# Optimization experiments

Measured on AMD Instinct MI355X. Metric: run time of the kernel, lower is better.

Reference implementation:

```python
import math
import jax, jax.numpy as jnp
import numpy as np

S = 32.0
M1 = 1.0
M2 = 0.5
M3 = 0.0
MM = M2 * math.sin(math.pi - M2)
NUM_CLASSES = 100000
FEATURES = 512
BATCH = 512


def setup_inputs() -> dict:
    key = jax.random.key(0)
    k1, k2, k3 = jax.random.split(key, 3)
    inputs = jax.random.normal(k1, (BATCH, FEATURES), dtype=jnp.float32)
    labels = jax.random.randint(k2, (BATCH,), 0, NUM_CLASSES, dtype=jnp.int64)
    # xavier_uniform on [num_classes, features]
    limit = math.sqrt(6.0 / (NUM_CLASSES + FEATURES))
    weight = jax.random.uniform(k3, (NUM_CLASSES, FEATURES), minval=-limit, maxval=limit, dtype=jnp.float32)
    return {"inputs": inputs, "labels": labels, "weight": weight}


def reference(inputs, labels, weight):
    # L2 normalize (torch F.normalize uses eps=1e-12 clamp on norm)
    inp_n = inputs / jnp.maximum(jnp.linalg.norm(inputs, axis=1, keepdims=True), 1e-12)
    w_n = weight / jnp.maximum(jnp.linalg.norm(weight, axis=1, keepdims=True), 1e-12)
    cos_in = jnp.clip(inp_n @ w_n.T, -1.0 + 1e-6, 1.0 - 1e-6)  # [N, C]
    theta_in = jnp.arccos(cos_in)
    one_hot = jax.nn.one_hot(labels, NUM_CLASSES, dtype=cos_in.dtype)
    theta_out = theta_in + (theta_in * (M1 - 1.0) + M2) * one_hot
    cos_out = jnp.where(
        theta_out < math.pi,
        jnp.cos(theta_out) - M3 * one_hot,
        cos_in - MM * one_hot - M3 * one_hot,
    )
    outs = S * cos_out  # [N, C]
    # mean cross-entropy
    logp = jax.nn.log_softmax(outs, axis=1)
    n = jnp.arange(BATCH)
    loss = -jnp.mean(logp[n, labels])
    target_cos_in = cos_in[n, labels][:, None]
    target_theta_in = theta_in[n, labels][:, None]
    target_cos_out = cos_out[n, labels][:, None]
    return loss, outs, target_cos_in, target_theta_in, target_cos_out
```

## Files before the change

### kernel.cpp

```cpp
#include <hip/hip_runtime.h>
#include <stdint.h>

#define BATCH 512
#define FEAT 512
#define NCLS 100000
#define BM 128
#define BN 128
#define BK 64
#define NBLK_N 782
#define NBLK (NBLK_N * 4)
#define NCHUNK (NBLK_N * 2)
#define SCALE_S 32.0f
#define MARGIN 0.5f
#define MM_CONST 0.23971276930210156f
#define PI_F 3.14159265358979f

typedef unsigned int u32;
typedef unsigned short u16;
typedef __bf16 bf16x8 __attribute__((ext_vector_type(8)));
typedef float f32x4 __attribute__((ext_vector_type(4)));

__device__ __forceinline__ u16 f2bf(float f) {
  u32 u = __float_as_uint(f);
  u += 0x7fffu + ((u >> 16) & 1u);
  return (u16)(u >> 16);
}

__device__ __forceinline__ void async_copy16(const void* g, void* l) {
  __builtin_amdgcn_global_load_lds((const __attribute__((address_space(1))) u32*)g,
                                   (__attribute__((address_space(3))) u32*)l,
                                   16, 0, 0);
}

__device__ __forceinline__ float block_reduce_sum(float v, float* sbuf) {
  for (int off = 1; off < 64; off <<= 1) v += __shfl_xor(v, off, 64);
  int wid = threadIdx.x >> 6, lane = threadIdx.x & 63;
  __syncthreads();
  if (lane == 0) sbuf[wid] = v;
  __syncthreads();
  return sbuf[0] + sbuf[1] + sbuf[2] + sbuf[3];
}

__global__ __launch_bounds__(256) void norm_all_kernel(const float* __restrict__ inputs,
                                                       const float* __restrict__ weight,
                                                       u16* __restrict__ dstA,
                                                       u16* __restrict__ dstB) {
  const int lane = threadIdx.x & 63;
  const int gw = (blockIdx.x * 256 + threadIdx.x) >> 6;
  const int nw = gridDim.x * 4;
  for (int row = gw; row < BATCH + NCLS; row += nw) {
    const float* src;
    u16* dst;
    if (row < BATCH) {
      src = inputs + (size_t)row * FEAT;
      dst = dstA + (size_t)row * FEAT;
    } else {
      src = weight + (size_t)(row - BATCH) * FEAT;
      dst = dstB + (size_t)(row - BATCH) * FEAT;
    }
    const float4* p4 = (const float4*)src;
    float4 a = p4[lane];
    float4 b = p4[lane + 64];
    float ss = a.x * a.x + a.y * a.y + a.z * a.z + a.w * a.w +
               b.x * b.x + b.y * b.y + b.z * b.z + b.w * b.w;
#pragma unroll
    for (int off = 1; off < 64; off <<= 1) ss += __shfl_xor(ss, off, 64);
    float inv = 1.0f / fmaxf(sqrtf(ss), 1e-12f);
    ushort4 oa, ob;
    oa.x = f2bf(a.x * inv); oa.y = f2bf(a.y * inv);
    oa.z = f2bf(a.z * inv); oa.w = f2bf(a.w * inv);
    ob.x = f2bf(b.x * inv); ob.y = f2bf(b.y * inv);
    ob.z = f2bf(b.z * inv); ob.w = f2bf(b.w * inv);
    ((ushort4*)dst)[lane] = oa;
    ((ushort4*)dst)[lane + 64] = ob;
  }
}

__global__ __launch_bounds__(256) void gemm_kernel(const u16* __restrict__ A,
                                                   const u16* __restrict__ B,
                                                   const int* __restrict__ labels,
                                                   float* __restrict__ outs,
                                                   float* __restrict__ partials) {
  __shared__ __align__(16) u16 sA[2][BM * BK];
  __shared__ __align__(16) u16 sB[2][BN * BK];
  __shared__ int sLab[BM];

  const int tid = threadIdx.x;
  const int lane = tid & 63;
  const int wid = tid >> 6;
  const int waveM = wid >> 1, waveN = wid & 1;
  const int orig = blockIdx.x;
  const int L = (orig & 7) * (NBLK / 8) + (orig >> 3);
  const int bm = L & 3, bn = L >> 2;
  const int quad = lane >> 4, l15 = lane & 15;

  if (tid < BM) sLab[tid] = labels[bm * BM + tid];

  const u16* gA[4];
  const u16* gB[4];
#pragma unroll
  for (int rd = 0; rd < 4; ++rd) {
    int idx = rd * 256 + tid;
    int r = idx >> 3;
    int cb = (idx & 7) ^ (r & 7);
    gA[rd] = A + (size_t)(bm * BM + r) * FEAT + cb * 8;
    int brow = bn * BN + r;
    if (brow >= NCLS) brow = NCLS - 1;
    gB[rd] = B + (size_t)brow * FEAT + cb * 8;
  }

#define STAGE(buf, kt)                                      \
  do {                                                      \
    _Pragma("unroll") for (int rd = 0; rd < 4; ++rd) {      \
      int li = (rd * 256 + tid) * 8;                        \
      async_copy16(gA[rd] + (kt)*BK, &sA[buf][li]);         \
      async_copy16(gB[rd] + (kt)*BK, &sB[buf][li]);         \
    }                                                       \
  } while (0)

  f32x4 acc[4][4] = {};

  STAGE(0, 0);
  __syncthreads();

  int cur = 0;
#pragma unroll
  for (int kt = 0; kt < FEAT / BK; ++kt) {
    if (kt < FEAT / BK - 1) {
      STAGE(cur ^ 1, kt + 1);
      asm volatile("s_waitcnt vmcnt(8)" ::: "memory");
    } else {
      asm volatile("s_waitcnt vmcnt(0)" ::: "memory");
    }
    asm volatile("s_barrier" ::: "memory");
#pragma unroll
    for (int ks = 0; ks < 2; ++ks) {
      int j0 = ks * 4 + quad;
      bf16x8 aF[4], bF[4];
#pragma unroll
      for (int mi = 0; mi < 4; ++mi) {
        int r = waveM * 64 + mi * 16 + l15;
        aF[mi] = *(const bf16x8*)&sA[cur][(r * 8 + (j0 ^ (r & 7))) * 8];
      }
#pragma unroll
      for (int ni = 0; ni < 4; ++ni) {
        int r = waveN * 64 + ni * 16 + l15;
        bF[ni] = *(const bf16x8*)&sB[cur][(r * 8 + (j0 ^ (r & 7))) * 8];
      }
#pragma unroll
      for (int mi = 0; mi < 4; ++mi)
#pragma unroll
        for (int ni = 0; ni < 4; ++ni)
          acc[mi][ni] = __builtin_amdgcn_mfma_f32_16x16x32_bf16(aF[mi], bF[ni],
                                                                acc[mi][ni], 0, 0, 0);
    }
    asm volatile("s_barrier" ::: "memory");
    cur ^= 1;
  }
#undef STAGE

#pragma unroll
  for (int mi = 0; mi < 4; ++mi) {
#pragma unroll
    for (int reg = 0; reg < 4; ++reg) {
      int rloc = waveM * 64 + mi * 16 + quad * 4 + reg;
      int rg = bm * BM + rloc;
      int lab = sLab[rloc];
      float vals[4];
      float rmax = -1e30f;
#pragma unroll
      for (int ni = 0; ni < 4; ++ni) {
        int cg = bn * BN + waveN * 64 + ni * 16 + l15;
        float v = acc[mi][ni][reg];
        v = fminf(fmaxf(v, -1.0f + 1e-6f), 1.0f - 1e-6f);
        if (cg == lab) {
          float th = acosf(v) + MARGIN;
          v = (th < PI_F) ? cosf(th) : (v - MM_CONST);
        }
        v *= SCALE_S;
        if (cg < NCLS)
          outs[(size_t)rg * NCLS + cg] = v;
        else
          v = -1e30f;
        vals[ni] = v;
        rmax = fmaxf(rmax, v);
      }
#pragma unroll
      for (int off = 1; off < 16; off <<= 1) rmax = fmaxf(rmax, __shfl_xor(rmax, off, 64));
      float rsum = 0.f;
#pragma unroll
      for (int ni = 0; ni < 4; ++ni) rsum += __expf(vals[ni] - rmax);
#pragma unroll
      for (int off = 1; off < 16; off <<= 1) rsum += __shfl_xor(rsum, off, 64);
      if (l15 == 0) {
        float* p = partials + ((size_t)rg * NCHUNK + (bn * 2 + waveN)) * 2;
        p[0] = rmax;
        p[1] = rsum;
      }
    }
  }
}

__global__ __launch_bounds__(256) void combine_kernel(const float* __restrict__ partials,
                                                      const float* __restrict__ outs,
                                                      const int* __restrict__ labels,
                                                      float* __restrict__ loss_r) {
  int r = blockIdx.x, tid = threadIdx.x;
  const float* p = partials + (size_t)r * NCHUNK * 2;
  float m = -1e30f, l = 0.f;
  for (int i = tid; i < NCHUNK; i += 256) {
    float mi = p[2 * i], li = p[2 * i + 1];
    if (mi > m) { l = l * __expf(m - mi) + li; m = mi; }
    else l += li * __expf(mi - m);
  }
  for (int off = 1; off < 64; off <<= 1) {
    float mo = __shfl_xor(m, off, 64);
    float lo = __shfl_xor(l, off, 64);
    if (mo > m) { l = l * __expf(m - mo) + lo; m = mo; }
    else l += lo * __expf(mo - m);
  }
  __shared__ float sm[4], sl[4];
  int wv = tid >> 6, lane = tid & 63;
  if (lane == 0) { sm[wv] = m; sl[wv] = l; }
  __syncthreads();
  if (tid == 0) {
    for (int w = 1; w < 4; ++w) {
      float mo = sm[w], lo = sl[w];
      if (mo > m) { l = l * __expf(m - mo) + lo; m = mo; }
      else l += lo * __expf(mo - m);
    }
    float lse = m + logf(l);
    loss_r[r] = lse - outs[(size_t)r * NCLS + labels[r]];
  }
}

__global__ __launch_bounds__(256) void loss_kernel(const float* __restrict__ loss_r,
                                                   float* __restrict__ out0) {
  __shared__ float sbuf[4];
  float v = loss_r[threadIdx.x] + loss_r[threadIdx.x + 256];
  float s = block_reduce_sum(v, sbuf);
  if (threadIdx.x == 0) out0[0] = s * (1.0f / BATCH);
}

__global__ __launch_bounds__(256) void targets_kernel(const float* __restrict__ inputs,
                                                      const int* __restrict__ labels,
                                                      const float* __restrict__ weight,
                                                      float* __restrict__ tdst) {
  __shared__ float sbuf[4];
  int r = blockIdx.x, t = threadIdx.x;
  int lab = labels[r];
  const float2* px = (const float2*)(inputs + (size_t)r * FEAT);
  const float2* pw = (const float2*)(weight + (size_t)lab * FEAT);
  float2 x = px[t], w = pw[t];
  float dot = block_reduce_sum(x.x * w.x + x.y * w.y, sbuf);
  float sx = block_reduce_sum(x.x * x.x + x.y * x.y, sbuf);
  float sw = block_reduce_sum(w.x * w.x + w.y * w.y, sbuf);
  if (t == 0) {
    float inv = 1.0f / (fmaxf(sqrtf(sx), 1e-12f) * fmaxf(sqrtf(sw), 1e-12f));
    float ci = fminf(fmaxf(dot * inv, -1.0f + 1e-6f), 1.0f - 1e-6f);
    float th = acosf(ci);
    float t2 = th + MARGIN;
    float co = (t2 < PI_F) ? cosf(t2) : (ci - MM_CONST);
    tdst[r] = ci;
    tdst[BATCH + r] = th;
    tdst[2 * BATCH + r] = co;
  }
}

extern "C" void kernel_launch(void* const* d_in, const int* in_sizes, int n_in,
                              void* d_out, int out_size, void* d_ws, size_t ws_size,
                              hipStream_t stream) {
  const float* inputs = (const float*)d_in[0];
  const int* labels = (const int*)d_in[1];
  const float* weight = (const float*)d_in[2];
  float* out = (float*)d_out;
  float* outs = out + 1;
  float* tdst = out + 1 + (size_t)BATCH * NCLS;

  char* ws = (char*)d_ws;
  u16* wsA = (u16*)ws;
  u16* wsB = (u16*)(ws + 524288);
  float* partials = (float*)(ws + 524288 + 102400000);
  float* loss_r = (float*)(ws + 524288 + 102400000 + (size_t)BATCH * NCHUNK * 2 * 4);

  norm_all_kernel<<<2048, 256, 0, stream>>>(inputs, weight, wsA, wsB);
  gemm_kernel<<<NBLK, 256, 0, stream>>>(wsA, wsB, labels, outs, partials);
  combine_kernel<<<BATCH, 256, 0, stream>>>(partials, outs, labels, loss_r);
  loss_kernel<<<1, 256, 0, stream>>>(loss_r, out);
  targets_kernel<<<BATCH, 256, 0, stream>>>(inputs, labels, weight, tdst);
}
```

Before: 561.0 us.

## Load A fragments directly from global, shrink LDS, fuse loss and target kernels

```diff
diff --git a/kernel.cpp b/kernel.cpp
--- a/kernel.cpp
+++ b/kernel.cpp
@@ -44,7 +44,9 @@
 __global__ __launch_bounds__(256) void norm_all_kernel(const float* __restrict__ inputs,
                                                        const float* __restrict__ weight,
                                                        u16* __restrict__ dstA,
-                                                       u16* __restrict__ dstB) {
+                                                       u16* __restrict__ dstB,
+                                                       float* __restrict__ out0) {
+  if (blockIdx.x == 0 && threadIdx.x == 0) out0[0] = 0.0f;
   const int lane = threadIdx.x & 63;
   const int gw = (blockIdx.x * 256 + threadIdx.x) >> 6;
   const int nw = gridDim.x * 4;
@@ -76,13 +78,13 @@
   }
 }
 
-__global__ __launch_bounds__(256) void gemm_kernel(const u16* __restrict__ A,
-                                                   const u16* __restrict__ B,
-                                                   const int* __restrict__ labels,
-                                                   float* __restrict__ outs,
-                                                   float* __restrict__ partials) {
-  __shared__ __align__(16) u16 sA[2][BM * BK];
-  __shared__ __align__(16) u16 sB[2][BN * BK];
+__global__ __launch_bounds__(256, 3) void gemm_kernel(const u16* __restrict__ A,
+                                                      const u16* __restrict__ B,
+                                                      const int* __restrict__ labels,
+                                                      float* __restrict__ outs,
+                                                      float* __restrict__ partials) {
+  __shared__ __align__(16) u16 sB0[BN * BK];
+  __shared__ __align__(16) u16 sB1[BN * BK];
   __shared__ int sLab[BM];
 
   const int tid = threadIdx.x;
@@ -96,68 +98,71 @@
 
   if (tid < BM) sLab[tid] = labels[bm * BM + tid];
 
-  const u16* gA[4];
   const u16* gB[4];
 #pragma unroll
   for (int rd = 0; rd < 4; ++rd) {
     int idx = rd * 256 + tid;
     int r = idx >> 3;
     int cb = (idx & 7) ^ (r & 7);
-    gA[rd] = A + (size_t)(bm * BM + r) * FEAT + cb * 8;
     int brow = bn * BN + r;
     if (brow >= NCLS) brow = NCLS - 1;
     gB[rd] = B + (size_t)brow * FEAT + cb * 8;
   }
-
-#define STAGE(buf, kt)                                      \
-  do {                                                      \
-    _Pragma("unroll") for (int rd = 0; rd < 4; ++rd) {      \
-      int li = (rd * 256 + tid) * 8;                        \
-      async_copy16(gA[rd] + (kt)*BK, &sA[buf][li]);         \
-      async_copy16(gB[rd] + (kt)*BK, &sB[buf][li]);         \
-    }                                                       \
+  const u16* gA = A + (size_t)(bm * BM + waveM * 64 + l15) * FEAT;
+
+  f32x4 acc[4][4] = {};
+
+#define STAGE_B(SBUF, KT)                                         \
+  do {                                                            \
+    _Pragma("unroll") for (int rd = 0; rd < 4; ++rd)              \
+        async_copy16(gB[rd] + (KT)*BK, &(SBUF)[(rd * 256 + tid) * 8]); \
   } while (0)
 
-  f32x4 acc[4][4] = {};
-
-  STAGE(0, 0);
-  __syncthreads();
-
-  int cur = 0;
-#pragma unroll
-  for (int kt = 0; kt < FEAT / BK; ++kt) {
-    if (kt < FEAT / BK - 1) {
-      STAGE(cur ^ 1, kt + 1);
-      asm volatile("s_waitcnt vmcnt(8)" ::: "memory");
-    } else {
-      asm volatile("s_waitcnt vmcnt(0)" ::: "memory");
-    }
-    asm volatile("s_barrier" ::: "memory");
-#pragma unroll
-    for (int ks = 0; ks < 2; ++ks) {
-      int j0 = ks * 4 + quad;
-      bf16x8 aF[4], bF[4];
-#pragma unroll
-      for (int mi = 0; mi < 4; ++mi) {
-        int r = waveM * 64 + mi * 16 + l15;
-        aF[mi] = *(const bf16x8*)&sA[cur][(r * 8 + (j0 ^ (r & 7))) * 8];
-      }
-#pragma unroll
-      for (int ni = 0; ni < 4; ++ni) {
-        int r = waveN * 64 + ni * 16 + l15;
-        bF[ni] = *(const bf16x8*)&sB[cur][(r * 8 + (j0 ^ (r & 7))) * 8];
-      }
-#pragma unroll
-      for (int mi = 0; mi < 4; ++mi)
-#pragma unroll
-        for (int ni = 0; ni < 4; ++ni)
-          acc[mi][ni] = __builtin_amdgcn_mfma_f32_16x16x32_bf16(aF[mi], bF[ni],
-                                                                acc[mi][ni], 0, 0, 0);
-    }
-    asm volatile("s_barrier" ::: "memory");
-    cur ^= 1;
-  }
-#undef STAGE
+#define K_STEP(SBUF_CUR, SBUF_NXT, KT, LAST)                                     \
+  do {                                                                           \
+    bf16x8 aF[4][2];                                                             \
+    _Pragma("unroll") for (int mi = 0; mi < 4; ++mi)                             \
+        _Pragma("unroll") for (int ks = 0; ks < 2; ++ks)                         \
+            aF[mi][ks] = *(const bf16x8*)(gA + (size_t)mi * 16 * FEAT +          \
+                                          (KT)*BK + (ks * 4 + quad) * 8);        \
+    __builtin_amdgcn_sched_barrier(0);      \
+    if (!(LAST)) {                                                               \
+      STAGE_B(SBUF_NXT, (KT) + 1);                                              \
+           \
+      asm volatile("s_waitcnt vmcnt(12)" ::: "memory");                          \
+    } else {                                                                     \
+      asm volatile("s_waitcnt vmcnt(8)" ::: "memory");            \
+    }                                                                            \
+    asm volatile("s_barrier" ::: "memory");      \
+    _Pragma("unroll") for (int ks = 0; ks < 2; ++ks) {                           \
+      int j0 = ks * 4 + quad;                                                    \
+      bf16x8 bF[4];                                                              \
+      _Pragma("unroll") for (int ni = 0; ni < 4; ++ni) {                         \
+        int r = waveN * 64 + ni * 16 + l15;                                      \
+        bF[ni] = *(const bf16x8*)&(SBUF_CUR)[(r * 8 + (j0 ^ (r & 7))) * 8];     \
+      }                                                                          \
+      _Pragma("unroll") for (int mi = 0; mi < 4; ++mi)                           \
+          _Pragma("unroll") for (int ni = 0; ni < 4; ++ni)                       \
+              acc[mi][ni] = __builtin_amdgcn_mfma_f32_16x16x32_bf16(             \
+                  aF[mi][ks], bF[ni], acc[mi][ni], 0, 0, 0);                     \
+    }                                                                            \
+    asm volatile("s_barrier" ::: "memory");   \
+  } while (0)
+
+  STAGE_B(sB0, 0);
+  __syncthreads();
+
+  K_STEP(sB0, sB1, 0, false);
+  K_STEP(sB1, sB0, 1, false);
+  K_STEP(sB0, sB1, 2, false);
+  K_STEP(sB1, sB0, 3, false);
+  K_STEP(sB0, sB1, 4, false);
+  K_STEP(sB1, sB0, 5, false);
+  K_STEP(sB0, sB1, 6, false);
+  K_STEP(sB1, sB0, 7, true);
+
+#undef K_STEP
+#undef STAGE_B
 
 #pragma unroll
   for (int mi = 0; mi < 4; ++mi) {
@@ -204,8 +209,22 @@
 __global__ __launch_bounds__(256) void combine_kernel(const float* __restrict__ partials,
                                                       const float* __restrict__ outs,
                                                       const int* __restrict__ labels,
-                                                      float* __restrict__ loss_r) {
+                                                      const float* __restrict__ inputs,
+                                                      const float* __restrict__ weight,
+                                                      float* __restrict__ out0,
+                                                      float* __restrict__ tdst) {
+  __shared__ float sbuf[4];
+  __shared__ float smx[4], slx[4];
   int r = blockIdx.x, tid = threadIdx.x;
+  int lab = labels[r];
+
+  const float2* px = (const float2*)(inputs + (size_t)r * FEAT);
+  const float2* pw = (const float2*)(weight + (size_t)lab * FEAT);
+  float2 x = px[tid], w = pw[tid];
+  float dot = block_reduce_sum(x.x * w.x + x.y * w.y, sbuf);
+  float sx = block_reduce_sum(x.x * x.x + x.y * x.y, sbuf);
+  float sw = block_reduce_sum(w.x * w.x + w.y * w.y, sbuf);
+
   const float* p = partials + (size_t)r * NCHUNK * 2;
   float m = -1e30f, l = 0.f;
   for (int i = tid; i < NCHUNK; i += 256) {
@@ -219,43 +238,19 @@
     if (mo > m) { l = l * __expf(m - mo) + lo; m = mo; }
     else l += lo * __expf(mo - m);
   }
-  __shared__ float sm[4], sl[4];
   int wv = tid >> 6, lane = tid & 63;
-  if (lane == 0) { sm[wv] = m; sl[wv] = l; }
+  if (lane == 0) { smx[wv] = m; slx[wv] = l; }
   __syncthreads();
   if (tid == 0) {
-    for (int w = 1; w < 4; ++w) {
-      float mo = sm[w], lo = sl[w];
+    for (int wq = 1; wq < 4; ++wq) {
+      float mo = smx[wq], lo = slx[wq];
       if (mo > m) { l = l * __expf(m - mo) + lo; m = mo; }
       else l += lo * __expf(mo - m);
     }
     float lse = m + logf(l);
-    loss_r[r] = lse - outs[(size_t)r * NCLS + labels[r]];
-  }
-}
-
-__global__ __launch_bounds__(256) void loss_kernel(const float* __restrict__ loss_r,
-                                                   float* __restrict__ out0) {
-  __shared__ float sbuf[4];
-  float v = loss_r[threadIdx.x] + loss_r[threadIdx.x + 256];
-  float s = block_reduce_sum(v, sbuf);
-  if (threadIdx.x == 0) out0[0] = s * (1.0f / BATCH);
-}
-
-__global__ __launch_bounds__(256) void targets_kernel(const float* __restrict__ inputs,
-                                                      const int* __restrict__ labels,
-                                                      const float* __restrict__ weight,
-                                                      float* __restrict__ tdst) {
-  __shared__ float sbuf[4];
-  int r = blockIdx.x, t = threadIdx.x;
-  int lab = labels[r];
-  const float2* px = (const float2*)(inputs + (size_t)r * FEAT);
-  const float2* pw = (const float2*)(weight + (size_t)lab * FEAT);
-  float2 x = px[t], w = pw[t];
-  float dot = block_reduce_sum(x.x * w.x + x.y * w.y, sbuf);
-  float sx = block_reduce_sum(x.x * x.x + x.y * x.y, sbuf);
-  float sw = block_reduce_sum(w.x * w.x + w.y * w.y, sbuf);
-  if (t == 0) {
+    float tgt = outs[(size_t)r * NCLS + lab];
+    atomicAdd(out0, (lse - tgt) * (1.0f / BATCH));
+
     float inv = 1.0f / (fmaxf(sqrtf(sx), 1e-12f) * fmaxf(sqrtf(sw), 1e-12f));
     float ci = fminf(fmaxf(dot * inv, -1.0f + 1e-6f), 1.0f - 1e-6f);
     float th = acosf(ci);
@@ -281,11 +276,8 @@
   u16* wsA = (u16*)ws;
   u16* wsB = (u16*)(ws + 524288);
   float* partials = (float*)(ws + 524288 + 102400000);
-  float* loss_r = (float*)(ws + 524288 + 102400000 + (size_t)BATCH * NCHUNK * 2 * 4);
-
-  norm_all_kernel<<<2048, 256, 0, stream>>>(inputs, weight, wsA, wsB);
+
+  norm_all_kernel<<<2048, 256, 0, stream>>>(inputs, weight, wsA, wsB, out);
   gemm_kernel<<<NBLK, 256, 0, stream>>>(wsA, wsB, labels, outs, partials);
-  combine_kernel<<<BATCH, 256, 0, stream>>>(partials, outs, labels, loss_r);
-  loss_kernel<<<1, 256, 0, stream>>>(loss_r, out);
-  targets_kernel<<<BATCH, 256, 0, stream>>>(inputs, labels, weight, tdst);
-}
+  combine_kernel<<<BATCH, 256, 0, stream>>>(partials, outs, labels, inputs, weight, out, tdst);
+}
```

Result: faster. 507.3 us (-9.6%).
